# Performance work log

Hardware: AMD Instinct MI355X
Metric: run time of the kernel (lower is better)

## Reference

```python
import jax, jax.numpy as jnp
import numpy as np


def setup_inputs() -> dict:
    key = jax.random.key(0)
    k1, k2, k3, k4, k5 = jax.random.split(key, 5)
    N_IN, N_OUT = 200000, 400000
    K, P = 27, 50000  # kernel volume (3^3), pairs per kernel offset
    CIN, COUT = 64, 32
    feats = jax.random.normal(k1, (N_IN, CIN), dtype=jnp.float32)
    weight = jax.random.normal(k2, (K, CIN, COUT), dtype=jnp.float32) * (1.0 / np.sqrt(CIN * K))
    bias = jax.random.normal(k3, (COUT,), dtype=jnp.float32) * 0.01
    in_idx = jax.random.randint(k4, (K, P), 0, N_IN, dtype=jnp.int32)
    out_idx = jax.random.randint(k5, (K, P), 0, N_OUT, dtype=jnp.int32)
    return {"feats": feats, "weight": weight, "bias": bias,
            "in_idx": in_idx, "out_idx": out_idx, "n_out": N_OUT}


def reference(feats, weight, bias, in_idx, out_idx, n_out):
    # Rulebook-driven sparse inverse conv3d: gather -> per-offset GEMM -> scatter-add.
    K, P = in_idx.shape
    cout = weight.shape[-1]
    gathered = feats[in_idx]                               # [K, P, Cin]
    contrib = jnp.einsum('kpc,kco->kpo', gathered, weight)  # [K, P, Cout]
    out = jnp.zeros((n_out, cout), dtype=feats.dtype)
    out = out.at[out_idx.reshape(-1)].add(contrib.reshape(-1, cout))
    return out + bias
```

## Files before the change

kernel.cpp:

```cpp
#include <hip/hip_runtime.h>

#define CIN 64
#define COUT 32

typedef __attribute__((ext_vector_type(8))) short bf16x8;
typedef __attribute__((ext_vector_type(4))) float f32x4;

__device__ inline ushort f2bf(float x) {
    union { float f; unsigned u; } v; v.f = x;
    unsigned r = v.u + 0x7fff + ((v.u >> 16) & 1);
    return (ushort)(r >> 16);
}

__global__ __launch_bounds__(256) void cvt_kernel(
    const float* __restrict__ in, ushort* __restrict__ outb, int n4)
{
    int i = blockIdx.x * blockDim.x + threadIdx.x;
    if (i < n4) {
        float4 f = reinterpret_cast<const float4*>(in)[i];
        ushort4 u;
        u.x = f2bf(f.x); u.y = f2bf(f.y); u.z = f2bf(f.z); u.w = f2bf(f.w);
        reinterpret_cast<ushort4*>(outb)[i] = u;
    }
}

__global__ __launch_bounds__(256) void zero16_kernel(uint4* __restrict__ p, int n16)
{
    int i = blockIdx.x * blockDim.x + threadIdx.x;
    if (i < n16) p[i] = uint4{0u, 0u, 0u, 0u};
}

__global__ __launch_bounds__(256) void mfma_scatter_pk_kernel(
    const ushort* __restrict__ featsb,
    const float* __restrict__ weight,
    const int* __restrict__ in_idx,
    const int* __restrict__ out_idx,
    ushort* __restrict__ outh,
    int P, int ntiles, int waves_per_k)
{
    const int k    = blockIdx.y;
    const int lane = threadIdx.x & 63;
    const int wav  = blockIdx.x * (blockDim.x >> 6) + (threadIdx.x >> 6);
    const int col  = lane & 15;
    const int kch  = lane >> 4;

    bf16x8 bfrag[2][2];
    const float* __restrict__ Wk = weight + (long)k * CIN * COUT;
    #pragma unroll
    for (int ks = 0; ks < 2; ++ks)
        #pragma unroll
        for (int h = 0; h < 2; ++h) {
            bf16x8 t;
            #pragma unroll
            for (int e = 0; e < 8; ++e)
                t[e] = (short)f2bf(Wk[(ks * 32 + kch * 8 + e) * COUT + 2 * col + h]);
            bfrag[ks][h] = t;
        }

    const int base = k * P;
    for (int tile = wav; tile < ntiles; tile += waves_per_k) {
        const int p0 = tile << 4;
        const int pA = min(p0 + col, P - 1);
        const int row = in_idx[base + pA];

        const ushort* __restrict__ ar = featsb + (long)row * CIN + kch * 8;
        bf16x8 a0 = *reinterpret_cast<const bf16x8*>(ar);
        bf16x8 a1 = *reinterpret_cast<const bf16x8*>(ar + 32);

        f32x4 acc0 = {0.f, 0.f, 0.f, 0.f};
        f32x4 acc1 = {0.f, 0.f, 0.f, 0.f};
        acc0 = __builtin_amdgcn_mfma_f32_16x16x32_bf16(a0, bfrag[0][0], acc0, 0, 0, 0);
        acc0 = __builtin_amdgcn_mfma_f32_16x16x32_bf16(a1, bfrag[1][0], acc0, 0, 0, 0);
        acc1 = __builtin_amdgcn_mfma_f32_16x16x32_bf16(a0, bfrag[0][1], acc1, 0, 0, 0);
        acc1 = __builtin_amdgcn_mfma_f32_16x16x32_bf16(a1, bfrag[1][1], acc1, 0, 0, 0);

        #pragma unroll
        for (int r = 0; r < 4; ++r) {
            const int prow = p0 + kch * 4 + r;
            if (prow < P) {
                const int orow = out_idx[base + prow];
                union { _Float16 h[2]; unsigned u; } pk;
                pk.h[0] = (_Float16)acc0[r];
                pk.h[1] = (_Float16)acc1[r];
                const ushort* dst = outh + (long)orow * COUT + 2 * col;
                asm volatile("global_atomic_pk_add_f16 %0, %1, off"
                             :: "v"((unsigned long long)dst), "v"(pk.u)
                             : "memory");
            }
        }
    }
}

__global__ __launch_bounds__(256) void finalize_kernel(
    const unsigned* __restrict__ outh_u, const float* __restrict__ bias,
    float* __restrict__ out, int n4)
{
    int i = blockIdx.x * blockDim.x + threadIdx.x;
    if (i < n4) {
        unsigned u0 = outh_u[2 * i], u1 = outh_u[2 * i + 1];
        int ch = (i * 4) & (COUT - 1);
        union { unsigned u; _Float16 h[2]; } a, b;
        a.u = u0; b.u = u1;
        float4 o;
        o.x = (float)a.h[0] + bias[ch + 0];
        o.y = (float)a.h[1] + bias[ch + 1];
        o.z = (float)b.h[0] + bias[ch + 2];
        o.w = (float)b.h[1] + bias[ch + 3];
        reinterpret_cast<float4*>(out)[i] = o;
    }
}


__global__ __launch_bounds__(256) void bias_init_kernel(
    float* __restrict__ out, const float* __restrict__ bias, int total)
{
    int i = (blockIdx.x * blockDim.x + threadIdx.x) * 4;
    if (i < total) {
        int ch = i & (COUT - 1);
        float4 b;
        b.x = bias[ch + 0]; b.y = bias[ch + 1];
        b.z = bias[ch + 2]; b.w = bias[ch + 3];
        *reinterpret_cast<float4*>(out + i) = b;
    }
}

__global__ __launch_bounds__(256) void scatter_gemm_kernel(
    const float* __restrict__ feats,
    const float* __restrict__ weight,
    const int* __restrict__ in_idx,
    const int* __restrict__ out_idx,
    float* __restrict__ out,
    int P, int n_groups)
{
    const int k        = blockIdx.y;
    const int lane     = threadIdx.x & 31;
    const int group_id = blockIdx.x * (blockDim.x >> 5) + (threadIdx.x >> 5);

    float w[CIN];
    const float* __restrict__ Wk = weight + (long)k * CIN * COUT;
    #pragma unroll
    for (int c = 0; c < CIN; ++c) w[c] = Wk[c * COUT + lane];

    const int base    = k * P;
    const int nchunks = (P + 31) >> 5;
    for (int ch = group_id; ch < nchunks; ch += n_groups) {
        const int p0 = ch << 5;
        const int n  = min(32, P - p0);
        int my_in = 0, my_out = 0;
        if (lane < n) {
            my_in  = in_idx[base + p0 + lane];
            my_out = out_idx[base + p0 + lane];
        }
        #pragma unroll 4
        for (int j = 0; j < n; ++j) {
            const int in = __shfl(my_in,  j, 32);
            const int o  = __shfl(my_out, j, 32);
            const float4* __restrict__ fr =
                reinterpret_cast<const float4*>(feats + (long)in * CIN);
            float acc = 0.0f;
            #pragma unroll
            for (int c4 = 0; c4 < CIN / 4; ++c4) {
                float4 f = fr[c4];
                acc += f.x * w[4 * c4 + 0];
                acc += f.y * w[4 * c4 + 1];
                acc += f.z * w[4 * c4 + 2];
                acc += f.w * w[4 * c4 + 3];
            }
            atomicAdd(out + (long)o * COUT + lane, acc);
        }
    }
}


extern "C" void kernel_launch(void* const* d_in, const int* in_sizes, int n_in,
                              void* d_out, int out_size, void* d_ws, size_t ws_size,
                              hipStream_t stream) {
    const float* feats   = (const float*)d_in[0];
    const float* weight  = (const float*)d_in[1];
    const float* bias    = (const float*)d_in[2];
    const int*   in_idx  = (const int*)d_in[3];
    const int*   out_idx = (const int*)d_in[4];
    float*       out     = (float*)d_out;

    const int K      = in_sizes[1] / (CIN * COUT);
    const int P      = in_sizes[3] / K;
    const int n_feat = in_sizes[0];
    const int n_out  = out_size / COUT;

    size_t featsb_bytes = (size_t)n_feat * 2;
    size_t outh_off     = (featsb_bytes + 255) & ~(size_t)255;
    size_t need         = outh_off + (size_t)out_size * 2;

    if (need > ws_size || (out_size & 3) != 0) {
        int total4 = out_size / 4;
        bias_init_kernel<<<(total4 + 255) / 256, 256, 0, stream>>>(out, bias, out_size);
        const int blocks_x = 96;
        const int n_groups = blocks_x * (256 / 32);
        dim3 grid(blocks_x, K);
        scatter_gemm_kernel<<<grid, 256, 0, stream>>>(feats, weight, in_idx, out_idx,
                                                      out, P, n_groups);
        return;
    }

    ushort* featsb = (ushort*)d_ws;
    ushort* outh   = (ushort*)((char*)d_ws + outh_off);

    cvt_kernel<<<(n_feat / 4 + 255) / 256, 256, 0, stream>>>(feats, featsb, n_feat / 4);
    {
        int n16 = (out_size * 2) / 16;
        zero16_kernel<<<(n16 + 255) / 256, 256, 0, stream>>>((uint4*)outh, n16);
    }

    {
        const int ntiles      = (P + 15) / 16;
        const int blocks_x    = 196;
        const int waves_per_k = blocks_x * (256 / 64);
        dim3 grid(blocks_x, K);
        mfma_scatter_pk_kernel<<<grid, 256, 0, stream>>>(featsb, weight, in_idx,
                                                         out_idx, outh, P, ntiles,
                                                         waves_per_k);
    }

    finalize_kernel<<<(out_size / 4 + 255) / 256, 256, 0, stream>>>(
        (const unsigned*)outh, bias, out, out_size / 4);
}
```

Before: 108.7 us.

## Fuse bf16 conversion into gather and transpose outputs via LDS for per-row atomics

Drops the separate feats-to-bf16 conversion pass: the MFMA kernel now gathers fp32 feature rows directly and converts them to bf16 in registers. It also stages the MFMA accumulators through a per-wave LDS slab so each lane holds four consecutive packed-f16 pairs of one output row, issuing four atomics at adjacent offsets instead of atomics spread across rows. This saves a full read/write pass over feats and reduces the number of out_idx loads, but each random gather now moves twice the bytes, since feats is reused about 6.75 times across offsets. There is no barrier between the LDS writes and reads within a wave, so correctness relies on in-wave ordering.

```diff
diff --git a/kernel.cpp b/kernel.cpp
--- a/kernel.cpp
+++ b/kernel.cpp
@@ -12,37 +12,29 @@
     return (ushort)(r >> 16);
 }
 
-__global__ __launch_bounds__(256) void cvt_kernel(
-    const float* __restrict__ in, ushort* __restrict__ outb, int n4)
-{
-    int i = blockIdx.x * blockDim.x + threadIdx.x;
-    if (i < n4) {
-        float4 f = reinterpret_cast<const float4*>(in)[i];
-        ushort4 u;
-        u.x = f2bf(f.x); u.y = f2bf(f.y); u.z = f2bf(f.z); u.w = f2bf(f.w);
-        reinterpret_cast<ushort4*>(outb)[i] = u;
-    }
-}
-
 __global__ __launch_bounds__(256) void zero16_kernel(uint4* __restrict__ p, int n16)
 {
     int i = blockIdx.x * blockDim.x + threadIdx.x;
     if (i < n16) p[i] = uint4{0u, 0u, 0u, 0u};
 }
 
-__global__ __launch_bounds__(256) void mfma_scatter_pk_kernel(
-    const ushort* __restrict__ featsb,
+__global__ __launch_bounds__(256) void mfma_scatter_pk2_kernel(
+    const float* __restrict__ feats,
     const float* __restrict__ weight,
     const int* __restrict__ in_idx,
     const int* __restrict__ out_idx,
     ushort* __restrict__ outh,
     int P, int ntiles, int waves_per_k)
 {
+    __shared__ unsigned ldsT[4 * 320];
+
     const int k    = blockIdx.y;
     const int lane = threadIdx.x & 63;
-    const int wav  = blockIdx.x * (blockDim.x >> 6) + (threadIdx.x >> 6);
+    const int wblk = threadIdx.x >> 6;
+    const int wav  = blockIdx.x * 4 + wblk;
     const int col  = lane & 15;
     const int kch  = lane >> 4;
+    unsigned* __restrict__ slab = &ldsT[wblk * 320];
 
     bf16x8 bfrag[2][2];
     const float* __restrict__ Wk = weight + (long)k * CIN * COUT;
@@ -57,15 +49,30 @@
             bfrag[ks][h] = t;
         }
 
+    const int r_abs = lane & 15;
+    const int cbase = (lane >> 4) * 4;
+
     const int base = k * P;
     for (int tile = wav; tile < ntiles; tile += waves_per_k) {
         const int p0 = tile << 4;
-        const int pA = min(p0 + col, P - 1);
+
+        const int pA  = min(p0 + col, P - 1);
         const int row = in_idx[base + pA];
-
-        const ushort* __restrict__ ar = featsb + (long)row * CIN + kch * 8;
-        bf16x8 a0 = *reinterpret_cast<const bf16x8*>(ar);
-        bf16x8 a1 = *reinterpret_cast<const bf16x8*>(ar + 32);
+        const float* __restrict__ ar = feats + (long)row * CIN + kch * 8;
+        float4 f0 = *reinterpret_cast<const float4*>(ar);
+        float4 f1 = *reinterpret_cast<const float4*>(ar + 4);
+        float4 f2 = *reinterpret_cast<const float4*>(ar + 32);
+        float4 f3 = *reinterpret_cast<const float4*>(ar + 36);
+
+        bf16x8 a0, a1;
+        a0[0] = (short)f2bf(f0.x); a0[1] = (short)f2bf(f0.y);
+        a0[2] = (short)f2bf(f0.z); a0[3] = (short)f2bf(f0.w);
+        a0[4] = (short)f2bf(f1.x); a0[5] = (short)f2bf(f1.y);
+        a0[6] = (short)f2bf(f1.z); a0[7] = (short)f2bf(f1.w);
+        a1[0] = (short)f2bf(f2.x); a1[1] = (short)f2bf(f2.y);
+        a1[2] = (short)f2bf(f2.z); a1[3] = (short)f2bf(f2.w);
+        a1[4] = (short)f2bf(f3.x); a1[5] = (short)f2bf(f3.y);
+        a1[6] = (short)f2bf(f3.z); a1[7] = (short)f2bf(f3.w);
 
         f32x4 acc0 = {0.f, 0.f, 0.f, 0.f};
         f32x4 acc1 = {0.f, 0.f, 0.f, 0.f};
@@ -76,17 +83,28 @@
 
         #pragma unroll
         for (int r = 0; r < 4; ++r) {
-            const int prow = p0 + kch * 4 + r;
-            if (prow < P) {
-                const int orow = out_idx[base + prow];
-                union { _Float16 h[2]; unsigned u; } pk;
-                pk.h[0] = (_Float16)acc0[r];
-                pk.h[1] = (_Float16)acc1[r];
-                const ushort* dst = outh + (long)orow * COUT + 2 * col;
-                asm volatile("global_atomic_pk_add_f16 %0, %1, off"
-                             :: "v"((unsigned long long)dst), "v"(pk.u)
-                             : "memory");
-            }
+            union { _Float16 h[2]; unsigned u; } pk;
+            pk.h[0] = (_Float16)acc0[r];
+            pk.h[1] = (_Float16)acc1[r];
+            slab[(4 * kch + r) * 20 + col] = pk.u;
+        }
+
+        uint4 vals = *reinterpret_cast<const uint4*>(&slab[r_abs * 20 + cbase]);
+
+        const int prow = p0 + r_abs;
+        if (prow < P) {
+            const int orow = out_idx[base + prow];
+            unsigned long long addr = (unsigned long long)outh
+                                    + (unsigned long long)orow * (COUT * 2)
+                                    + (unsigned)(cbase * 4);
+            asm volatile("global_atomic_pk_add_f16 %0, %1, off"
+                         :: "v"(addr), "v"(vals.x) : "memory");
+            asm volatile("global_atomic_pk_add_f16 %0, %1, off offset:4"
+                         :: "v"(addr), "v"(vals.y) : "memory");
+            asm volatile("global_atomic_pk_add_f16 %0, %1, off offset:8"
+                         :: "v"(addr), "v"(vals.z) : "memory");
+            asm volatile("global_atomic_pk_add_f16 %0, %1, off offset:12"
+                         :: "v"(addr), "v"(vals.w) : "memory");
         }
     }
 }
@@ -182,16 +200,12 @@
     const int*   out_idx = (const int*)d_in[4];
     float*       out     = (float*)d_out;
 
-    const int K      = in_sizes[1] / (CIN * COUT);
-    const int P      = in_sizes[3] / K;
-    const int n_feat = in_sizes[0];
-    const int n_out  = out_size / COUT;
-
-    size_t featsb_bytes = (size_t)n_feat * 2;
-    size_t outh_off     = (featsb_bytes + 255) & ~(size_t)255;
-    size_t need         = outh_off + (size_t)out_size * 2;
-
-    if (need > ws_size || (out_size & 3) != 0) {
+    const int K = in_sizes[1] / (CIN * COUT);
+    const int P = in_sizes[3] / K;
+
+    size_t need = (size_t)out_size * 2;
+
+    if (need > ws_size || (out_size & 7) != 0) {
         int total4 = out_size / 4;
         bias_init_kernel<<<(total4 + 255) / 256, 256, 0, stream>>>(out, bias, out_size);
         const int blocks_x = 96;
@@ -202,10 +216,8 @@
         return;
     }
 
-    ushort* featsb = (ushort*)d_ws;
-    ushort* outh   = (ushort*)((char*)d_ws + outh_off);
-
-    cvt_kernel<<<(n_feat / 4 + 255) / 256, 256, 0, stream>>>(feats, featsb, n_feat / 4);
+    ushort* outh = (ushort*)d_ws;
+
     {
         int n16 = (out_size * 2) / 16;
         zero16_kernel<<<(n16 + 255) / 256, 256, 0, stream>>>((uint4*)outh, n16);
@@ -214,11 +226,11 @@
     {
         const int ntiles      = (P + 15) / 16;
         const int blocks_x    = 196;
-        const int waves_per_k = blocks_x * (256 / 64);
+        const int waves_per_k = blocks_x * 4;
         dim3 grid(blocks_x, K);
-        mfma_scatter_pk_kernel<<<grid, 256, 0, stream>>>(featsb, weight, in_idx,
-                                                         out_idx, outh, P, ntiles,
-                                                         waves_per_k);
+        mfma_scatter_pk2_kernel<<<grid, 256, 0, stream>>>(feats, weight, in_idx,
+                                                          out_idx, outh, P, ntiles,
+                                                          waves_per_k);
     }
 
     finalize_kernel<<<(out_size / 4 + 255) / 256, 256, 0, stream>>>(
```

Result: slower. 305.5 us (+181.1%).
